# Performance work log

Hardware: AMD Instinct MI355X
Metric: run time of the kernel (lower is better)

The kernel has to match this reference:

```python
import jax, jax.numpy as jnp
import numpy as np

N_NODES = 100000
IN_CH, HID_CH, OUT_CH = 128, 256, 128
N_EDGES = 1600000


def setup_inputs() -> dict:
    key = jax.random.key(0)
    ks = jax.random.split(key, 12)
    x = jax.random.normal(ks[0], (N_NODES, IN_CH), dtype=jnp.float32)
    edge_index = jax.random.randint(ks[1], (2, N_EDGES), 0, N_NODES, dtype=jnp.int32)
    s1 = 1.0 / np.sqrt(IN_CH)
    s2 = 1.0 / np.sqrt(HID_CH)
    return {
        "x": x,
        "edge_index": edge_index,
        "eps1": jnp.zeros((), jnp.float32),
        "W1a": jax.random.uniform(ks[2], (IN_CH, HID_CH), jnp.float32, -s1, s1),
        "b1a": jax.random.uniform(ks[3], (HID_CH,), jnp.float32, -s1, s1),
        "W1b": jax.random.uniform(ks[4], (HID_CH, HID_CH), jnp.float32, -s2, s2),
        "b1b": jax.random.uniform(ks[5], (HID_CH,), jnp.float32, -s2, s2),
        "eps2": jnp.zeros((), jnp.float32),
        "W2a": jax.random.uniform(ks[6], (HID_CH, HID_CH), jnp.float32, -s2, s2),
        "b2a": jax.random.uniform(ks[7], (HID_CH,), jnp.float32, -s2, s2),
        "W2b": jax.random.uniform(ks[8], (HID_CH, OUT_CH), jnp.float32, -s2, s2),
        "b2b": jax.random.uniform(ks[9], (OUT_CH,), jnp.float32, -s2, s2),
    }


def _gin_conv(x, src, dst, eps, Wa, ba, Wb, bb):
    # sum-aggregate source features into destinations: [N, d]
    agg = jax.ops.segment_sum(x[src], dst, num_segments=N_NODES)
    h = (1.0 + eps) * x + agg
    h = jax.nn.relu(h @ Wa + ba)
    return h @ Wb + bb


def reference(x, edge_index, eps1, W1a, b1a, W1b, b1b, eps2, W2a, b2a, W2b, b2b):
    src, dst = edge_index[0], edge_index[1]
    h = _gin_conv(x, src, dst, eps1, W1a, b1a, W1b, b1b)
    h = jax.nn.relu(h)
    out = _gin_conv(h, src, dst, eps2, W2a, b2a, W2b, b2b)
    return out
```

## Files before the change

kernel.cpp:

```cpp
#include <hip/hip_runtime.h>

#define N_NODES 100000
#define N_EDGES 1600000
#define NB 782
#define SC_BLK 256

typedef __attribute__((ext_vector_type(8))) short short8;
typedef __attribute__((ext_vector_type(4))) float float4e;

#define GLDS16(g, l)                                                   \
  __builtin_amdgcn_global_load_lds(                                    \
      (const __attribute__((address_space(1))) unsigned int*)(g),      \
      (__attribute__((address_space(3))) unsigned int*)(l), 16, 0, 0)

__device__ __forceinline__ unsigned short f2bf(float f) {
  unsigned u = __float_as_uint(f);
  u += 0x7FFFu + ((u >> 16) & 1u);
  return (unsigned short)(u >> 16);
}
__device__ __forceinline__ float bf2f(unsigned short h) {
  return __uint_as_float(((unsigned)h) << 16);
}

__global__ __launch_bounds__(256) void histA_k(const int* __restrict__ dst,
                                               int* __restrict__ bh, int nE) {
  __shared__ int h[NB];
  const int blk = blockIdx.x, tid = threadIdx.x;
  for (int b = tid; b < NB; b += 256) h[b] = 0;
  __syncthreads();
  const int epb = (nE + SC_BLK - 1) / SC_BLK;
  const int i1 = min(blk * epb + epb, nE);
  for (int i = blk * epb + tid; i < i1; i += 256)
    atomicAdd(&h[dst[i] >> 7], 1);
  __syncthreads();
  for (int b = tid; b < NB; b += 256) bh[b * SC_BLK + blk] = h[b];
}

__global__ __launch_bounds__(256) void scanW_k(int* __restrict__ bh,
                                               int* __restrict__ tot) {
  const int b = blockIdx.x * 4 + (threadIdx.x >> 6);
  const int lane = threadIdx.x & 63;
  if (b >= NB) return;
  const int base = b * SC_BLK + lane * 4;
  int v[4];
#pragma unroll
  for (int j = 0; j < 4; ++j) v[j] = bh[base + j];
  int ls = v[0] + v[1] + v[2] + v[3];
  int x = ls;
  for (int off = 1; off < 64; off <<= 1) {
    int y = __shfl_up(x, off);
    if (lane >= off) x += y;
  }
  int run = x - ls;
#pragma unroll
  for (int j = 0; j < 4; ++j) {
    int t = v[j];
    bh[base + j] = run;
    run += t;
  }
  if (lane == 63) tot[b] = run;
}

__global__ __launch_bounds__(1024) void scanB2_k(const int* __restrict__ tot,
                                                 int* __restrict__ bucketStart) {
  __shared__ int sm[1024];
  const int tid = threadIdx.x;
  int v = (tid < NB) ? tot[tid] : 0;
  sm[tid] = v;
  __syncthreads();
  for (int off = 1; off < 1024; off <<= 1) {
    int t = (tid >= off) ? sm[tid - off] : 0;
    __syncthreads();
    sm[tid] += t;
    __syncthreads();
  }
  if (tid < NB) bucketStart[tid] = sm[tid] - v;
  if (tid == NB - 1) bucketStart[NB] = sm[tid];
}

__global__ __launch_bounds__(256) void scatter2_k(
    const int* __restrict__ src, const int* __restrict__ dst,
    const int* __restrict__ bucketStart, const int* __restrict__ bh,
    unsigned int* __restrict__ packed, int nE) {
  __shared__ int cur[NB];
  const int blk = blockIdx.x, tid = threadIdx.x;
  for (int b = tid; b < NB; b += 256)
    cur[b] = bucketStart[b] + bh[b * SC_BLK + blk];
  __syncthreads();
  const int epb = (nE + SC_BLK - 1) / SC_BLK;
  const int i1 = min(blk * epb + epb, nE);
  for (int i = blk * epb + tid; i < i1; i += 256) {
    int d = dst[i];
    int s = src[i];
    int p = atomicAdd(&cur[d >> 7], 1);
    packed[p] = ((unsigned)s << 7) | (unsigned)(d & 127);
  }
}

__global__ __launch_bounds__(256) void fillB_k(
    const int* __restrict__ bucketStart, const unsigned int* __restrict__ packed,
    int* __restrict__ rowEnd, int* __restrict__ sortedSrc, int nNodes) {
  __shared__ int cnt[128];
  __shared__ int cur[128];
  const int b = blockIdx.x;
  const int tid = threadIdx.x;
  const int s0 = bucketStart[b];
  const int ne = bucketStart[b + 1] - s0;
  if (tid < 128) cnt[tid] = 0;
  __syncthreads();
  for (int i = tid; i < ne; i += 256)
    atomicAdd(&cnt[packed[s0 + i] & 127u], 1);
  __syncthreads();
  int v = (tid < 128) ? cnt[tid] : 0;
  for (int off = 1; off < 128; off <<= 1) {
    int t = (tid < 128 && tid >= off) ? cnt[tid - off] : 0;
    __syncthreads();
    if (tid < 128) cnt[tid] += t;
    __syncthreads();
  }
  if (tid < 128) {
    cur[tid] = s0 + cnt[tid] - v;
    int node = b * 128 + tid;
    if (node < nNodes) rowEnd[node] = s0 + cnt[tid];
  }
  __syncthreads();
  for (int i = tid; i < ne; i += 256) {
    unsigned p = packed[s0 + i];
    int idx = atomicAdd(&cur[p & 127u], 1);
    sortedSrc[idx] = (int)(p >> 7);
  }
}

__global__ __launch_bounds__(256) void wprep_k(
    const float* __restrict__ W, unsigned short* __restrict__ th,
    unsigned short* __restrict__ tl, int K, int N) {
  int i = blockIdx.x * blockDim.x + threadIdx.x;
  if (i < K * N) {
    int k = i / N, n = i % N;
    float v = W[i];
    unsigned short h = f2bf(v);
    unsigned short l = f2bf(v - bf2f(h));
    th[(long)n * K + k] = h;
    tl[(long)n * K + k] = l;
  }
}

__global__ __launch_bounds__(256) void xprep_k(const float* __restrict__ x,
                                               unsigned short* __restrict__ xh,
                                               int n) {
  int i = blockIdx.x * blockDim.x + threadIdx.x;
  if (i < n) xh[i] = f2bf(x[i]);
}

template <bool XF32>
__global__ __launch_bounds__(256) void agg_s_k(
    const unsigned short* __restrict__ feat_h, const float* __restrict__ xf,
    const unsigned short* __restrict__ xh, const unsigned short* __restrict__ xl,
    const float* __restrict__ epsp, const int* __restrict__ rowEnd,
    const int* __restrict__ sortedSrc, unsigned short* __restrict__ oh,
    unsigned short* __restrict__ ol, int M, int S, int off) {
  constexpr int V = 2;
  const int lane = threadIdx.x & 63;
  const int w = (int)((blockIdx.x * blockDim.x + threadIdx.x) >> 6);
  if (w >= M) return;
  const int start = w ? rowEnd[w - 1] : 0;
  const int end = rowEnd[w];
  const int c0 = lane * V + off;

  float acc[V] = {};
  int e = start;
  for (; e + 8 <= end; e += 8) {
    int si[8];
#pragma unroll
    for (int q = 0; q < 8; ++q) si[q] = sortedSrc[e + q];
    ushort2 t[8];
#pragma unroll
    for (int q = 0; q < 8; ++q)
      t[q] = *(const ushort2*)(feat_h + (long)si[q] * S + c0);
#pragma unroll
    for (int q = 0; q < 8; ++q) {
      acc[0] += bf2f(t[q].x);
      acc[1] += bf2f(t[q].y);
    }
  }
  for (; e + 4 <= end; e += 4) {
    int s0 = sortedSrc[e + 0];
    int s1 = sortedSrc[e + 1];
    int s2 = sortedSrc[e + 2];
    int s3 = sortedSrc[e + 3];
    ushort2 a = *(const ushort2*)(feat_h + (long)s0 * S + c0);
    ushort2 b = *(const ushort2*)(feat_h + (long)s1 * S + c0);
    ushort2 c = *(const ushort2*)(feat_h + (long)s2 * S + c0);
    ushort2 d = *(const ushort2*)(feat_h + (long)s3 * S + c0);
    acc[0] += bf2f(a.x) + bf2f(b.x) + bf2f(c.x) + bf2f(d.x);
    acc[1] += bf2f(a.y) + bf2f(b.y) + bf2f(c.y) + bf2f(d.y);
  }
  for (; e < end; ++e) {
    ushort2 a = *(const ushort2*)(feat_h + (long)sortedSrc[e] * S + c0);
    acc[0] += bf2f(a.x);
    acc[1] += bf2f(a.y);
  }

  const float s = 1.0f + epsp[0];
  float xv[V];
  if constexpr (XF32) {
#pragma unroll
    for (int v = 0; v < V; ++v) xv[v] = xf[(long)w * S + c0 + v];
  } else {
#pragma unroll
    for (int v = 0; v < V; ++v)
      xv[v] = bf2f(xh[(long)w * S + c0 + v]) + bf2f(xl[(long)w * S + c0 + v]);
  }

  unsigned short hv[V], lv[V];
#pragma unroll
  for (int v = 0; v < V; ++v) {
    float res = fmaf(s, xv[v], acc[v]);
    hv[v] = f2bf(res);
    lv[v] = f2bf(res - bf2f(hv[v]));
  }
  *(ushort2*)&oh[(long)w * S + c0] = make_ushort2(hv[0], hv[1]);
  *(ushort2*)&ol[(long)w * S + c0] = make_ushort2(lv[0], lv[1]);
}

__device__ __forceinline__ short8 lds_rd(const unsigned short* base, int r,
                                         int q) {
  int L = r * 64 + q * 16;
  int P = L ^ (((L >> 7) & 7) << 4);
  return *(const short8*)((const char*)base + P);
}

template <bool RELU, bool HILO>
__global__ __launch_bounds__(256, 2) void gemm128_k(
    const unsigned short* __restrict__ Ah, const unsigned short* __restrict__ Al,
    const unsigned short* __restrict__ Bth, const unsigned short* __restrict__ Btl,
    const float* __restrict__ bias, float* __restrict__ outf,
    unsigned short* __restrict__ oh, unsigned short* __restrict__ ol,
    int M, int K, int NOUT) {
  __shared__ unsigned short Ash[128 * 32];
  __shared__ unsigned short Asl[128 * 32];
  __shared__ unsigned short Bsh[128 * 32];
  __shared__ unsigned short Bsl[128 * 32];

  const int tid = threadIdx.x;
  const int lane = tid & 63;
  const int wave = tid >> 6;
  const int l15 = lane & 15;
  const int quad = lane >> 4;
  const int wm = wave >> 1;
  const int wn = wave & 1;
  const int m0 = blockIdx.x * 128;
  const int n0 = blockIdx.y * 128;

  float4e acc[4][4];
#pragma unroll
  for (int i = 0; i < 4; ++i)
#pragma unroll
    for (int j = 0; j < 4; ++j) acc[i][j] = 0.0f;

  for (int k0 = 0; k0 < K; k0 += 32) {
#pragma unroll
    for (int h = 0; h < 2; ++h) {
      int c = h * 256 + tid;
      int P = c * 16;
      int L = P ^ (((P >> 7) & 7) << 4);
      int r = L >> 6;
      int q = (L >> 4) & 3;
      if (m0 + r < M) {
        long ga = (long)(m0 + r) * K + k0 + q * 8;
        GLDS16(Ah + ga, Ash + c * 8);
        GLDS16(Al + ga, Asl + c * 8);
      }
      long gb = (long)(n0 + r) * K + k0 + q * 8;
      GLDS16(Bth + gb, Bsh + c * 8);
      GLDS16(Btl + gb, Bsl + c * 8);
    }
    __syncthreads();

    short8 ah[4], al[4];
#pragma unroll
    for (int mi = 0; mi < 4; ++mi) {
      ah[mi] = lds_rd(Ash, wm * 64 + mi * 16 + l15, quad);
      al[mi] = lds_rd(Asl, wm * 64 + mi * 16 + l15, quad);
    }
#pragma unroll
    for (int ni = 0; ni < 4; ++ni) {
      short8 bh = lds_rd(Bsh, wn * 64 + ni * 16 + l15, quad);
      short8 bl = lds_rd(Bsl, wn * 64 + ni * 16 + l15, quad);
#pragma unroll
      for (int mi = 0; mi < 4; ++mi) {
        acc[mi][ni] =
            __builtin_amdgcn_mfma_f32_16x16x32_bf16(ah[mi], bh, acc[mi][ni], 0, 0, 0);
        acc[mi][ni] =
            __builtin_amdgcn_mfma_f32_16x16x32_bf16(ah[mi], bl, acc[mi][ni], 0, 0, 0);
        acc[mi][ni] =
            __builtin_amdgcn_mfma_f32_16x16x32_bf16(al[mi], bh, acc[mi][ni], 0, 0, 0);
      }
    }
    __syncthreads();
  }

#pragma unroll
  for (int mi = 0; mi < 4; ++mi) {
#pragma unroll
    for (int ni = 0; ni < 4; ++ni) {
      int col = n0 + wn * 64 + ni * 16 + l15;
      float bj = bias[col];
      int rbase = m0 + wm * 64 + mi * 16 + quad * 4;
#pragma unroll
      for (int r = 0; r < 4; ++r) {
        int row = rbase + r;
        if (row < M) {
          float v = acc[mi][ni][r] + bj;
          if constexpr (RELU) v = fmaxf(v, 0.0f);
          if constexpr (HILO) {
            unsigned short h = f2bf(v);
            oh[(long)row * NOUT + col] = h;
            ol[(long)row * NOUT + col] = f2bf(v - bf2f(h));
          } else {
            outf[(long)row * NOUT + col] = v;
          }
        }
      }
    }
  }
}

extern "C" void kernel_launch(void* const* d_in, const int* in_sizes, int n_in,
                              void* d_out, int out_size, void* d_ws, size_t ws_size,
                              hipStream_t stream) {
  const float* x    = (const float*)d_in[0];
  const int*   ei   = (const int*)d_in[1];
  const float* eps1 = (const float*)d_in[2];
  const float* W1a  = (const float*)d_in[3];
  const float* b1a  = (const float*)d_in[4];
  const float* W1b  = (const float*)d_in[5];
  const float* b1b  = (const float*)d_in[6];
  const float* eps2 = (const float*)d_in[7];
  const float* W2a  = (const float*)d_in[8];
  const float* b2a  = (const float*)d_in[9];
  const float* W2b  = (const float*)d_in[10];
  const float* b2b  = (const float*)d_in[11];
  float* out = (float*)d_out;

  const int* srcp = ei;
  const int* dstp = ei + N_EDGES;

  char* ws = (char*)d_ws;
  const size_t SZ = (size_t)N_NODES * 256 * sizeof(float);
  char* P1 = ws;
  char* P2 = ws + SZ;

  unsigned short* C1h = (unsigned short*)P1;
  unsigned short* C1l = C1h + (size_t)N_NODES * 128;
  unsigned short* xh  = C1l + (size_t)N_NODES * 128;
  unsigned short* T1h = (unsigned short*)P2;
  unsigned short* T1l = T1h + (size_t)N_NODES * 256;
  unsigned short* Hh = (unsigned short*)P1;
  unsigned short* Hl = Hh + (size_t)N_NODES * 256;
  unsigned short* C2h = (unsigned short*)P2;
  unsigned short* C2l = C2h + (size_t)N_NODES * 256;
  unsigned short* T2h = (unsigned short*)P1;
  unsigned short* T2l = T2h + (size_t)N_NODES * 256;
  unsigned short* W2bh = (unsigned short*)P2;
  unsigned short* W2bl = W2bh + 128 * 256;

  char* ob = (char*)d_out;
  int* rowEnd    = (int*)(ob + 400 * 1024);
  int* sortedSrc = (int*)(ob + 800 * 1024);
  size_t wofs = 7340032;
  unsigned short* W1ah = (unsigned short*)(ob + wofs);
  unsigned short* W1al = W1ah + 256 * 128;
  unsigned short* W1bh = (unsigned short*)(ob + wofs + 2 * 65536);
  unsigned short* W1bl = W1bh + 256 * 256;
  unsigned short* W2ah = (unsigned short*)(ob + wofs + 2 * 65536 + 2 * 131072);
  unsigned short* W2al = W2ah + 256 * 256;
  unsigned int* packed = (unsigned int*)(ob + 16 * 1024 * 1024);
  int* bucketStart = (int*)(ob + 28 * 1024 * 1024);
  int* bucketTot   = (int*)(ob + 28 * 1024 * 1024 + 8192);
  int* blockHist   = (int*)(ob + 30 * 1024 * 1024);

  dim3 blk(256);
  dim3 gAgg((N_NODES + 3) / 4);
  dim3 gW1((128 * 256 + 255) / 256);
  dim3 gW2((256 * 256 + 255) / 256);
  dim3 gXp((N_NODES * 128 + 255) / 256);
  dim3 gGemm2((N_NODES + 127) / 128, 2);
  dim3 gGemm1((N_NODES + 127) / 128, 1);

  histA_k<<<dim3(SC_BLK), blk, 0, stream>>>(dstp, blockHist, N_EDGES);
  scanW_k<<<dim3((NB + 3) / 4), blk, 0, stream>>>(blockHist, bucketTot);
  scanB2_k<<<1, dim3(1024), 0, stream>>>(bucketTot, bucketStart);
  scatter2_k<<<dim3(SC_BLK), blk, 0, stream>>>(srcp, dstp, bucketStart,
                                               blockHist, packed, N_EDGES);
  fillB_k<<<dim3(NB), blk, 0, stream>>>(bucketStart, packed, rowEnd, sortedSrc,
                                        N_NODES);
  xprep_k<<<gXp, blk, 0, stream>>>(x, xh, N_NODES * 128);
  wprep_k<<<gW1, blk, 0, stream>>>(W1a, W1ah, W1al, 128, 256);
  wprep_k<<<gW2, blk, 0, stream>>>(W1b, W1bh, W1bl, 256, 256);
  wprep_k<<<gW2, blk, 0, stream>>>(W2a, W2ah, W2al, 256, 256);

  agg_s_k<true><<<gAgg, blk, 0, stream>>>(
      xh, x, nullptr, nullptr, eps1, rowEnd, sortedSrc, C1h, C1l, N_NODES, 128, 0);
  gemm128_k<true, true><<<gGemm2, blk, 0, stream>>>(
      C1h, C1l, W1ah, W1al, b1a, nullptr, T1h, T1l, N_NODES, 128, 256);
  gemm128_k<true, true><<<gGemm2, blk, 0, stream>>>(
      T1h, T1l, W1bh, W1bl, b1b, nullptr, Hh, Hl, N_NODES, 256, 256);

  agg_s_k<false><<<gAgg, blk, 0, stream>>>(
      Hh, nullptr, Hh, Hl, eps2, rowEnd, sortedSrc, C2h, C2l, N_NODES, 256, 0);
  agg_s_k<false><<<gAgg, blk, 0, stream>>>(
      Hh, nullptr, Hh, Hl, eps2, rowEnd, sortedSrc, C2h, C2l, N_NODES, 256, 128);
  gemm128_k<true, true><<<gGemm2, blk, 0, stream>>>(
      C2h, C2l, W2ah, W2al, b2a, nullptr, T2h, T2l, N_NODES, 256, 256);
  wprep_k<<<gW1, blk, 0, stream>>>(W2b, W2bh, W2bl, 256, 128);
  gemm128_k<false, false><<<gGemm1, blk, 0, stream>>>(
      T2h, T2l, W2bh, W2bl, b2b, out, nullptr, nullptr, N_NODES, 256, 128);
}
```

Measured before the change: 662.7 us.

## Stage GEMM epilogue through LDS for coalesced stores and remap blocks per XCD

```diff
diff --git a/kernel.cpp b/kernel.cpp
--- a/kernel.cpp
+++ b/kernel.cpp
@@ -230,17 +230,20 @@
   return *(const short8*)((const char*)base + P);
 }
 
-template <bool RELU, bool HILO>
+#define MFMA_BF16 __builtin_amdgcn_mfma_f32_16x16x32_bf16
+
+template <int NY, bool RELU, bool HILO>
 __global__ __launch_bounds__(256, 2) void gemm128_k(
     const unsigned short* __restrict__ Ah, const unsigned short* __restrict__ Al,
     const unsigned short* __restrict__ Bth, const unsigned short* __restrict__ Btl,
     const float* __restrict__ bias, float* __restrict__ outf,
     unsigned short* __restrict__ oh, unsigned short* __restrict__ ol,
     int M, int K, int NOUT) {
-  __shared__ unsigned short Ash[128 * 32];
-  __shared__ unsigned short Asl[128 * 32];
-  __shared__ unsigned short Bsh[128 * 32];
-  __shared__ unsigned short Bsl[128 * 32];
+  __shared__ unsigned short Sm[16384];
+  unsigned short* Ash = Sm;
+  unsigned short* Asl = Sm + 4096;
+  unsigned short* Bsh = Sm + 8192;
+  unsigned short* Bsl = Sm + 12288;
 
   const int tid = threadIdx.x;
   const int lane = tid & 63;
@@ -249,8 +252,21 @@
   const int quad = lane >> 4;
   const int wm = wave >> 1;
   const int wn = wave & 1;
-  const int m0 = blockIdx.x * 128;
-  const int n0 = blockIdx.y * 128;
+
+  const int nwg = gridDim.x;
+  const int q8 = nwg >> 3, r8 = nwg & 7;
+  const int xcd = blockIdx.x & 7, idx = blockIdx.x >> 3;
+  const int lin =
+      (xcd < r8 ? xcd * (q8 + 1) : r8 * (q8 + 1) + (xcd - r8) * q8) + idx;
+  int bx, n0;
+  if (NY == 2) {
+    bx = lin >> 1;
+    n0 = (lin & 1) * 128;
+  } else {
+    bx = lin;
+    n0 = 0;
+  }
+  const int m0 = bx * 128;
 
   float4e acc[4][4];
 #pragma unroll
@@ -266,14 +282,13 @@
       int L = P ^ (((P >> 7) & 7) << 4);
       int r = L >> 6;
       int q = (L >> 4) & 3;
-      if (m0 + r < M) {
-        long ga = (long)(m0 + r) * K + k0 + q * 8;
-        GLDS16(Ah + ga, Ash + c * 8);
-        GLDS16(Al + ga, Asl + c * 8);
-      }
+      int ra = min(m0 + r, M - 1);
+      long ga = (long)ra * K + k0 + q * 8;
+      GLDS16(Ah + ga, &Ash[c * 8]);
+      GLDS16(Al + ga, &Asl[c * 8]);
       long gb = (long)(n0 + r) * K + k0 + q * 8;
-      GLDS16(Bth + gb, Bsh + c * 8);
-      GLDS16(Btl + gb, Bsl + c * 8);
+      GLDS16(Bth + gb, &Bsh[c * 8]);
+      GLDS16(Btl + gb, &Bsl[c * 8]);
     }
     __syncthreads();
 
@@ -289,35 +304,64 @@
       short8 bl = lds_rd(Bsl, wn * 64 + ni * 16 + l15, quad);
 #pragma unroll
       for (int mi = 0; mi < 4; ++mi) {
-        acc[mi][ni] =
-            __builtin_amdgcn_mfma_f32_16x16x32_bf16(ah[mi], bh, acc[mi][ni], 0, 0, 0);
-        acc[mi][ni] =
-            __builtin_amdgcn_mfma_f32_16x16x32_bf16(ah[mi], bl, acc[mi][ni], 0, 0, 0);
-        acc[mi][ni] =
-            __builtin_amdgcn_mfma_f32_16x16x32_bf16(al[mi], bh, acc[mi][ni], 0, 0, 0);
+        acc[mi][ni] = MFMA_BF16(ah[mi], bh, acc[mi][ni], 0, 0, 0);
+        acc[mi][ni] = MFMA_BF16(ah[mi], bl, acc[mi][ni], 0, 0, 0);
+        acc[mi][ni] = MFMA_BF16(al[mi], bh, acc[mi][ni], 0, 0, 0);
       }
     }
     __syncthreads();
   }
 
-#pragma unroll
-  for (int mi = 0; mi < 4; ++mi) {
+  if constexpr (HILO) {
+#pragma unroll
+    for (int pass = 0; pass < 2; ++pass) {
+#pragma unroll
+      for (int ni = 0; ni < 4; ++ni) {
+        int col = wn * 64 + ni * 16 + l15;
+        float bj = bias[n0 + col];
+#pragma unroll
+        for (int mi = 0; mi < 4; ++mi) {
+#pragma unroll
+          for (int r = 0; r < 4; ++r) {
+            int row = wm * 64 + mi * 16 + quad * 4 + r;
+            float v = acc[mi][ni][r] + bj;
+            if constexpr (RELU) v = fmaxf(v, 0.0f);
+            unsigned short hv = f2bf(v);
+            unsigned short wv = pass ? f2bf(v - bf2f(hv)) : hv;
+            int B = row * 256 + col * 2;
+            int SB = B ^ (((row >> 2) & 3) << 5);
+            *(unsigned short*)((char*)Sm + SB) = wv;
+          }
+        }
+      }
+      __syncthreads();
+      unsigned short* dst = pass ? ol : oh;
+#pragma unroll
+      for (int i = 0; i < 8; ++i) {
+        int li = i * 256 + tid;
+        int row = li >> 4, chk = li & 15;
+        int B = row * 256 + chk * 16;
+        int SB = B ^ (((row >> 2) & 3) << 5);
+        if (m0 + row < M)
+          *(short8*)&dst[(long)(m0 + row) * NOUT + n0 + chk * 8] =
+              *(const short8*)((const char*)Sm + SB);
+      }
+      __syncthreads();
+    }
+  } else {
 #pragma unroll
     for (int ni = 0; ni < 4; ++ni) {
       int col = n0 + wn * 64 + ni * 16 + l15;
       float bj = bias[col];
-      int rbase = m0 + wm * 64 + mi * 16 + quad * 4;
-#pragma unroll
-      for (int r = 0; r < 4; ++r) {
-        int row = rbase + r;
-        if (row < M) {
-          float v = acc[mi][ni][r] + bj;
-          if constexpr (RELU) v = fmaxf(v, 0.0f);
-          if constexpr (HILO) {
-            unsigned short h = f2bf(v);
-            oh[(long)row * NOUT + col] = h;
-            ol[(long)row * NOUT + col] = f2bf(v - bf2f(h));
-          } else {
+#pragma unroll
+      for (int mi = 0; mi < 4; ++mi) {
+        int rbase = m0 + wm * 64 + mi * 16 + quad * 4;
+#pragma unroll
+        for (int r = 0; r < 4; ++r) {
+          int row = rbase + r;
+          if (row < M) {
+            float v = acc[mi][ni][r] + bj;
+            if constexpr (RELU) v = fmaxf(v, 0.0f);
             outf[(long)row * NOUT + col] = v;
           }
         }
@@ -385,8 +429,8 @@
   dim3 gW1((128 * 256 + 255) / 256);
   dim3 gW2((256 * 256 + 255) / 256);
   dim3 gXp((N_NODES * 128 + 255) / 256);
-  dim3 gGemm2((N_NODES + 127) / 128, 2);
-  dim3 gGemm1((N_NODES + 127) / 128, 1);
+  dim3 gGemm2(((N_NODES + 127) / 128) * 2);
+  dim3 gGemm1((N_NODES + 127) / 128);
 
   histA_k<<<dim3(SC_BLK), blk, 0, stream>>>(dstp, blockHist, N_EDGES);
   scanW_k<<<dim3((NB + 3) / 4), blk, 0, stream>>>(blockHist, bucketTot);
@@ -402,18 +446,18 @@
 
   agg_s_k<true><<<gAgg, blk, 0, stream>>>(
       xh, x, nullptr, nullptr, eps1, rowEnd, sortedSrc, C1h, C1l, N_NODES, 128, 0);
-  gemm128_k<true, true><<<gGemm2, blk, 0, stream>>>(
+  gemm128_k<2, true, true><<<gGemm2, blk, 0, stream>>>(
       C1h, C1l, W1ah, W1al, b1a, nullptr, T1h, T1l, N_NODES, 128, 256);
-  gemm128_k<true, true><<<gGemm2, blk, 0, stream>>>(
+  gemm128_k<2, true, true><<<gGemm2, blk, 0, stream>>>(
       T1h, T1l, W1bh, W1bl, b1b, nullptr, Hh, Hl, N_NODES, 256, 256);
 
   agg_s_k<false><<<gAgg, blk, 0, stream>>>(
       Hh, nullptr, Hh, Hl, eps2, rowEnd, sortedSrc, C2h, C2l, N_NODES, 256, 0);
   agg_s_k<false><<<gAgg, blk, 0, stream>>>(
       Hh, nullptr, Hh, Hl, eps2, rowEnd, sortedSrc, C2h, C2l, N_NODES, 256, 128);
-  gemm128_k<true, true><<<gGemm2, blk, 0, stream>>>(
+  gemm128_k<2, true, true><<<gGemm2, blk, 0, stream>>>(
       C2h, C2l, W2ah, W2al, b2a, nullptr, T2h, T2l, N_NODES, 256, 256);
   wprep_k<<<gW1, blk, 0, stream>>>(W2b, W2bh, W2bl, 256, 128);
-  gemm128_k<false, false><<<gGemm1, blk, 0, stream>>>(
+  gemm128_k<1, false, false><<<gGemm1, blk, 0, stream>>>(
       T2h, T2l, W2bh, W2bl, b2b, out, nullptr, nullptr, N_NODES, 256, 128);
 }
```

After: 616.4 us, median of 2. 1.08x faster.
